# Kernel tuning notes

Hardware: AMD Instinct MI355X
Metric: run time of the kernel (lower is better)

## Reference

```python
import jax, jax.numpy as jnp
import numpy as np

N_QUERIES = 33_554_432  # 32M query points (128 MB fp32)
N_KNOTS = 1024          # interpolation table size


def setup_inputs() -> dict:
    key = jax.random.key(0)
    k1, k2, k3 = jax.random.split(key, 3)
    # queries spread slightly beyond the knot range to exercise clamping branches
    x = jax.random.uniform(k1, (N_QUERIES,), dtype=jnp.float32, minval=-0.1, maxval=1.1)
    # unsorted knots (module sorts them in __init__; reference sorts too)
    x_points = jax.random.uniform(k2, (N_KNOTS,), dtype=jnp.float32)
    y_points = jax.random.normal(k3, (N_KNOTS,), dtype=jnp.float32)
    return {"x": x, "x_points": x_points, "y_points": y_points}


def reference(x, x_points, y_points):
    # __init__: sort knots by x, permute y accordingly
    order = jnp.argsort(x_points)
    xp = x_points[order]
    yp = y_points[order]
    n = xp.shape[0]
    # torch.searchsorted default (right=False) == side='left'
    idx = jnp.searchsorted(xp, x, side="left")  # [N], int
    # interior lerp uses (idx-1, idx); clip so gathers are in-range
    hi = jnp.clip(idx, 1, n - 1)
    lo = hi - 1
    x1, x2 = xp[lo], xp[hi]
    y1, y2 = yp[lo], yp[hi]
    interp = y1 + (x - x1) * (y2 - y1) / (x2 - x1)
    # boundary clamps: idx==0 -> y[0]; idx>=n -> y[-1]
    out = jnp.where(idx == 0, yp[0], jnp.where(idx >= n, yp[-1], interp))
    return out
```

## Files before the change

kernel.cpp:

```cpp
#include <hip/hip_runtime.h>
#include <math.h>

#define NK 1024
#define NB 4096

#define WS_SXP   0
#define WS_META  1032
#define WS_QUAD  1040
#define WS_FTAB  5136

typedef float f4v __attribute__((ext_vector_type(4)));

__device__ __forceinline__ int bucket_of(float x, float lo, float scale) {
    float t = __fmul_rn(__fsub_rn(x, lo), scale);
    int b = (int)t;
    b = b < 0 ? 0 : b;
    b = b > (NB - 1) ? (NB - 1) : b;
    return b;
}

__global__ __launch_bounds__(1024) void setup_sort(
        const float* __restrict__ xp_in, const float* __restrict__ yp_in,
        float* __restrict__ wsf)
{
    __shared__ unsigned long long kl[NK];
    __shared__ float sxs[NK];
    __shared__ float sys[NK];

    const int t = threadIdx.x;

    float xv = xp_in[t];
    unsigned int fb  = __float_as_uint(xv);
    unsigned int k32 = (fb & 0x80000000u) ? ~fb : (fb | 0x80000000u);
    unsigned long long key = ((unsigned long long)k32 << 10) | (unsigned int)t;

    for (int k = 2; k <= NK; k <<= 1) {
        const bool dir = ((t & k) == 0);
        for (int j = k >> 1; j >= 64; j >>= 1) {
            kl[t] = key;
            __syncthreads();
            unsigned long long p = kl[t ^ j];
            __syncthreads();
            bool lower = ((t & j) == 0);
            bool wmin  = (dir == lower);
            unsigned long long mn = key < p ? key : p;
            unsigned long long mx = key < p ? p : key;
            key = wmin ? mn : mx;
        }
        for (int j = ((k >> 1) >= 64 ? 32 : (k >> 1)); j >= 1; j >>= 1) {
            unsigned long long p = __shfl_xor(key, j, 64);
            bool lower = ((t & j) == 0);
            bool wmin  = (dir == lower);
            unsigned long long mn = key < p ? key : p;
            unsigned long long mx = key < p ? p : key;
            key = wmin ? mn : mx;
        }
    }

    unsigned int idx0 = (unsigned int)(key & (NK - 1));
    unsigned int s32  = (unsigned int)(key >> 10);
    unsigned int xb   = (s32 & 0x80000000u) ? (s32 ^ 0x80000000u) : ~s32;
    float xs = __uint_as_float(xb);
    float ys = yp_in[idx0];
    sxs[t] = xs; sys[t] = ys;
    __syncthreads();

    float xn = (t < NK - 1) ? sxs[t + 1] : xs;
    float yn = (t < NK - 1) ? sys[t + 1] : ys;
    float slope = (t < NK - 1) ? (yn - ys) / (xn - xs) : 0.0f;

    wsf[WS_SXP + t] = xs;
    if (t < 8) wsf[WS_SXP + NK + t] = INFINITY;
    ((float4*)(wsf + WS_QUAD))[t] = make_float4(xs, ys, slope, 0.0f);
    if (t == 0) {
        float lo  = sxs[0];
        float xpN = sxs[NK - 1];
        float range = xpN - lo;
        wsf[WS_META + 0] = lo;
        wsf[WS_META + 1] = range * (1.0f / (float)NB);
        wsf[WS_META + 2] = (range > 0.0f) ? ((float)NB / range) : 0.0f;
        wsf[WS_META + 3] = sys[0];
        wsf[WS_META + 4] = sys[NK - 1];
        wsf[WS_META + 5] = xpN;
    }
}

__global__ __launch_bounds__(256) void setup_tables(float* __restrict__ wsf)
{
    __shared__ float sxp_s[NK];
    __shared__ int   lb[257];
    __shared__ float meta[6];

    const int tid = threadIdx.x;
    for (int i = tid; i < NK; i += 256) sxp_s[i] = wsf[WS_SXP + i];
    if (tid < 6) meta[tid] = wsf[WS_META + tid];
    __syncthreads();

    const float lo = meta[0], inv_scale = meta[1], scale = meta[2];
    const int base = blockIdx.x * 256;

    auto lbf = [&](int b) -> int {
        int loi = 0, hii = NK;
        while (loi < hii) {
            int mid = (loi + hii) >> 1;
            if (bucket_of(sxp_s[mid], lo, scale) < b) loi = mid + 1; else hii = mid;
        }
        return loi;
    };
    lb[tid] = lbf(base + tid);
    if (tid == 0) lb[256] = (base + 256 >= NB) ? NK : lbf(base + 256);
    __syncthreads();

    const int b   = base + tid;
    const int ib  = lb[tid];
    const int ib1 = lb[tid + 1];
    const int interior = ib1 - ib - (b == 0 ? 1 : 0) - (b == NB - 1 ? 1 : 0);

    float2 e;
    if (interior > 0) {
        e.x = __uint_as_float(0x7fc00000u);
        e.y = __uint_as_float((unsigned int)ib);
    } else {
        int hi = ib < 1 ? 1 : (ib > NK - 1 ? NK - 1 : ib);
        float4 qd = ((const float4*)(wsf + WS_QUAD))[hi - 1];
        float bl = __fmaf_rn((float)b, inv_scale, lo);
        e.x = qd.z;
        e.y = __fmaf_rn(bl - qd.x, qd.z, qd.y);
    }
    ((float2*)(wsf + WS_FTAB))[b] = e;
}

__device__ __forceinline__ float interp_one(
        float x, const float2* __restrict__ ftab, const float* __restrict__ sxp,
        const float4* __restrict__ gquads,
        float lo, float inv_scale, float scale, float xpN, float yp0, float ypN)
{
    int b = bucket_of(x, lo, scale);
    float2 e = ftab[b];
    float bl  = __fmaf_rn((float)b, inv_scale, lo);
    float res = __fmaf_rn(x - bl, e.x, e.y);
    if (__builtin_isnan(e.x) && x > lo && x <= xpN) {
        int j = (int)__float_as_uint(e.y);
        while (sxp[j] < x) ++j;
        int hi = j < 1 ? 1 : j;
        float4 qd = gquads[hi - 1];
        res = __fmaf_rn(x - qd.x, qd.z, qd.y);
    }
    res = (x <= lo)  ? yp0 : res;
    res = (x >  xpN) ? ypN : res;
    return res;
}

__global__ __launch_bounds__(512, 8) void interp_kernel(
        const f4v* __restrict__ xq, f4v* __restrict__ out,
        const float* __restrict__ wsf, int n4)
{
    __shared__ __align__(16) float2 ftab[NB];
    __shared__ float sxp_s[NK + 8];
    const int t = threadIdx.x;
    {
        const f4v* src = (const f4v*)(wsf + WS_FTAB);
        f4v*       dst = (f4v*)ftab;
        #pragma unroll
        for (int i = 0; i < 4; ++i) dst[t + 512 * i] = src[t + 512 * i];
        for (int i = t; i < NK + 8; i += 512) sxp_s[i] = wsf[WS_SXP + i];
    }
    const float lo        = wsf[WS_META + 0];
    const float inv_scale = wsf[WS_META + 1];
    const float scale     = wsf[WS_META + 2];
    const float yp0       = wsf[WS_META + 3];
    const float ypN       = wsf[WS_META + 4];
    const float xpN       = wsf[WS_META + 5];
    const float4* gquads  = (const float4*)(wsf + WS_QUAD);
    __syncthreads();

    int q = blockIdx.x * 512 + t;
    const int stride = gridDim.x * 512;
    for (; q + stride < n4; q += 2 * stride) {
        f4v xa = xq[q];
        f4v xb = xq[q + stride];
        f4v ra, rb;
        ra.x = interp_one(xa.x, ftab, sxp_s, gquads, lo, inv_scale, scale, xpN, yp0, ypN);
        ra.y = interp_one(xa.y, ftab, sxp_s, gquads, lo, inv_scale, scale, xpN, yp0, ypN);
        ra.z = interp_one(xa.z, ftab, sxp_s, gquads, lo, inv_scale, scale, xpN, yp0, ypN);
        ra.w = interp_one(xa.w, ftab, sxp_s, gquads, lo, inv_scale, scale, xpN, yp0, ypN);
        rb.x = interp_one(xb.x, ftab, sxp_s, gquads, lo, inv_scale, scale, xpN, yp0, ypN);
        rb.y = interp_one(xb.y, ftab, sxp_s, gquads, lo, inv_scale, scale, xpN, yp0, ypN);
        rb.z = interp_one(xb.z, ftab, sxp_s, gquads, lo, inv_scale, scale, xpN, yp0, ypN);
        rb.w = interp_one(xb.w, ftab, sxp_s, gquads, lo, inv_scale, scale, xpN, yp0, ypN);
        __builtin_nontemporal_store(ra, &out[q]);
        __builtin_nontemporal_store(rb, &out[q + stride]);
    }
    for (; q < n4; q += stride) {
        f4v xa = xq[q];
        f4v ra;
        ra.x = interp_one(xa.x, ftab, sxp_s, gquads, lo, inv_scale, scale, xpN, yp0, ypN);
        ra.y = interp_one(xa.y, ftab, sxp_s, gquads, lo, inv_scale, scale, xpN, yp0, ypN);
        ra.z = interp_one(xa.z, ftab, sxp_s, gquads, lo, inv_scale, scale, xpN, yp0, ypN);
        ra.w = interp_one(xa.w, ftab, sxp_s, gquads, lo, inv_scale, scale, xpN, yp0, ypN);
        __builtin_nontemporal_store(ra, &out[q]);
    }
}

extern "C" void kernel_launch(void* const* d_in, const int* in_sizes, int n_in,
                              void* d_out, int out_size, void* d_ws, size_t ws_size,
                              hipStream_t stream)
{
    const float* x  = (const float*)d_in[0];
    const float* xp = (const float*)d_in[1];
    const float* yp = (const float*)d_in[2];
    float* out = (float*)d_out;
    float* wsf = (float*)d_ws;

    setup_sort<<<1, 1024, 0, stream>>>(xp, yp, wsf);
    setup_tables<<<NB / 256, 256, 0, stream>>>(wsf);

    const int n4 = out_size / 4;
    interp_kernel<<<1024, 512, 0, stream>>>((const f4v*)x, (f4v*)out, wsf, n4);
}
```

Baseline: 262.3 us.

## Batch interpolation lookups for ILP and stage segment quads in LDS

Replaces the per-element interp_one with a templated batch routine. It issues all bucket-table loads for 8 (or 4) elements first, then runs three branch-free search steps before a residual while-loop. The per-segment quad table now lives in shared memory instead of being read from global memory, and the grid and launch bounds are reduced (768 blocks, min 6 waves). The aim is more memory-level and LDS-level parallelism and less divergent global gathers. The cost is extra LDS per block, which lowers resident blocks, plus unconditional LDS reads for lanes that need no search.

```diff
diff --git a/kernel.cpp b/kernel.cpp
--- a/kernel.cpp
+++ b/kernel.cpp
@@ -130,40 +130,71 @@
     ((float2*)(wsf + WS_FTAB))[b] = e;
 }
 
-__device__ __forceinline__ float interp_one(
-        float x, const float2* __restrict__ ftab, const float* __restrict__ sxp,
-        const float4* __restrict__ gquads,
+template<int U>
+__device__ __forceinline__ void interp_batch(
+        const float* xin, float* rout,
+        const float2* __restrict__ ftab, const float* __restrict__ sxp,
+        const float4* __restrict__ squad,
         float lo, float inv_scale, float scale, float xpN, float yp0, float ypN)
 {
-    int b = bucket_of(x, lo, scale);
-    float2 e = ftab[b];
-    float bl  = __fmaf_rn((float)b, inv_scale, lo);
-    float res = __fmaf_rn(x - bl, e.x, e.y);
-    if (__builtin_isnan(e.x) && x > lo && x <= xpN) {
-        int j = (int)__float_as_uint(e.y);
-        while (sxp[j] < x) ++j;
-        int hi = j < 1 ? 1 : j;
-        float4 qd = gquads[hi - 1];
-        res = __fmaf_rn(x - qd.x, qd.z, qd.y);
-    }
-    res = (x <= lo)  ? yp0 : res;
-    res = (x >  xpN) ? ypN : res;
-    return res;
-}
-
-__global__ __launch_bounds__(512, 8) void interp_kernel(
+    float2 e[U];
+    float  res[U];
+    int    j[U];
+    bool   fb[U];
+
+    #pragma unroll
+    for (int u = 0; u < U; ++u) {
+        int b = bucket_of(xin[u], lo, scale);
+        e[u] = ftab[b];
+        float bl = __fmaf_rn((float)b, inv_scale, lo);
+        res[u] = bl;
+    }
+    #pragma unroll
+    for (int u = 0; u < U; ++u) {
+        float bl = res[u];
+        res[u] = __fmaf_rn(xin[u] - bl, e[u].x, e[u].y);
+        fb[u]  = __builtin_isnan(e[u].x) && (xin[u] > lo) && (xin[u] <= xpN);
+        j[u]   = fb[u] ? (int)__float_as_uint(e[u].y) : 0;
+    }
+    #pragma unroll
+    for (int r = 0; r < 3; ++r) {
+        #pragma unroll
+        for (int u = 0; u < U; ++u) j[u] += (sxp[j[u]] < xin[u]) ? 1 : 0;
+    }
+    #pragma unroll
+    for (int u = 0; u < U; ++u)
+        while (fb[u] && sxp[j[u]] < xin[u]) ++j[u];
+    #pragma unroll
+    for (int u = 0; u < U; ++u) {
+        int hi = j[u] < 1 ? 1 : j[u];
+        float4 qd = squad[hi - 1];
+        float rf  = __fmaf_rn(xin[u] - qd.x, qd.z, qd.y);
+        res[u] = fb[u] ? rf : res[u];
+        res[u] = (xin[u] <= lo)  ? yp0 : res[u];
+        res[u] = (xin[u] >  xpN) ? ypN : res[u];
+        rout[u] = res[u];
+    }
+}
+
+__global__ __launch_bounds__(512, 6) void interp_kernel(
         const f4v* __restrict__ xq, f4v* __restrict__ out,
         const float* __restrict__ wsf, int n4)
 {
     __shared__ __align__(16) float2 ftab[NB];
-    __shared__ float sxp_s[NK + 8];
+    __shared__ __align__(16) float4 squad[NK];
+    __shared__ float sxp_s[NK];
     const int t = threadIdx.x;
     {
-        const f4v* src = (const f4v*)(wsf + WS_FTAB);
-        f4v*       dst = (f4v*)ftab;
-        #pragma unroll
-        for (int i = 0; i < 4; ++i) dst[t + 512 * i] = src[t + 512 * i];
-        for (int i = t; i < NK + 8; i += 512) sxp_s[i] = wsf[WS_SXP + i];
+        const f4v* fsrc = (const f4v*)(wsf + WS_FTAB);
+        f4v*       fdst = (f4v*)ftab;
+        #pragma unroll
+        for (int i = 0; i < 4; ++i) fdst[t + 512 * i] = fsrc[t + 512 * i];
+        const f4v* qsrc = (const f4v*)(wsf + WS_QUAD);
+        f4v*       qdst = (f4v*)squad;
+        #pragma unroll
+        for (int i = 0; i < 2; ++i) qdst[t + 512 * i] = qsrc[t + 512 * i];
+        #pragma unroll
+        for (int i = 0; i < 2; ++i) sxp_s[t + 512 * i] = wsf[WS_SXP + t + 512 * i];
     }
     const float lo        = wsf[WS_META + 0];
     const float inv_scale = wsf[WS_META + 1];
@@ -171,7 +202,6 @@
     const float yp0       = wsf[WS_META + 3];
     const float ypN       = wsf[WS_META + 4];
     const float xpN       = wsf[WS_META + 5];
-    const float4* gquads  = (const float4*)(wsf + WS_QUAD);
     __syncthreads();
 
     int q = blockIdx.x * 512 + t;
@@ -179,25 +209,22 @@
     for (; q + stride < n4; q += 2 * stride) {
         f4v xa = xq[q];
         f4v xb = xq[q + stride];
-        f4v ra, rb;
-        ra.x = interp_one(xa.x, ftab, sxp_s, gquads, lo, inv_scale, scale, xpN, yp0, ypN);
-        ra.y = interp_one(xa.y, ftab, sxp_s, gquads, lo, inv_scale, scale, xpN, yp0, ypN);
-        ra.z = interp_one(xa.z, ftab, sxp_s, gquads, lo, inv_scale, scale, xpN, yp0, ypN);
-        ra.w = interp_one(xa.w, ftab, sxp_s, gquads, lo, inv_scale, scale, xpN, yp0, ypN);
-        rb.x = interp_one(xb.x, ftab, sxp_s, gquads, lo, inv_scale, scale, xpN, yp0, ypN);
-        rb.y = interp_one(xb.y, ftab, sxp_s, gquads, lo, inv_scale, scale, xpN, yp0, ypN);
-        rb.z = interp_one(xb.z, ftab, sxp_s, gquads, lo, inv_scale, scale, xpN, yp0, ypN);
-        rb.w = interp_one(xb.w, ftab, sxp_s, gquads, lo, inv_scale, scale, xpN, yp0, ypN);
+        float xin[8] = {xa.x, xa.y, xa.z, xa.w, xb.x, xb.y, xb.z, xb.w};
+        float r8[8];
+        interp_batch<8>(xin, r8, ftab, sxp_s, squad,
+                        lo, inv_scale, scale, xpN, yp0, ypN);
+        f4v ra = {r8[0], r8[1], r8[2], r8[3]};
+        f4v rb = {r8[4], r8[5], r8[6], r8[7]};
         __builtin_nontemporal_store(ra, &out[q]);
         __builtin_nontemporal_store(rb, &out[q + stride]);
     }
     for (; q < n4; q += stride) {
         f4v xa = xq[q];
-        f4v ra;
-        ra.x = interp_one(xa.x, ftab, sxp_s, gquads, lo, inv_scale, scale, xpN, yp0, ypN);
-        ra.y = interp_one(xa.y, ftab, sxp_s, gquads, lo, inv_scale, scale, xpN, yp0, ypN);
-        ra.z = interp_one(xa.z, ftab, sxp_s, gquads, lo, inv_scale, scale, xpN, yp0, ypN);
-        ra.w = interp_one(xa.w, ftab, sxp_s, gquads, lo, inv_scale, scale, xpN, yp0, ypN);
+        float xin[4] = {xa.x, xa.y, xa.z, xa.w};
+        float r4[4];
+        interp_batch<4>(xin, r4, ftab, sxp_s, squad,
+                        lo, inv_scale, scale, xpN, yp0, ypN);
+        f4v ra = {r4[0], r4[1], r4[2], r4[3]};
         __builtin_nontemporal_store(ra, &out[q]);
     }
 }
@@ -216,5 +243,5 @@
     setup_tables<<<NB / 256, 256, 0, stream>>>(wsf);
 
     const int n4 = out_size / 4;
-    interp_kernel<<<1024, 512, 0, stream>>>((const f4v*)x, (f4v*)out, wsf, n4);
-}
+    interp_kernel<<<768, 512, 0, stream>>>((const f4v*)x, (f4v*)out, wsf, n4);
+}
```

Result: no change. 259.5 us (-1.1%).

## Resolve single-knot buckets directly via float4 table entries and restructure interp loop

Applied to the files above, without the earlier changes.

Widens the per-bucket lookup table to float4 so a bucket holding exactly one knot stores the knot position, its y, and the slopes on either side. Queries in such buckets pick a slope with one compare instead of taking the divergent linear-scan fallback. Only buckets with two or more knots keep the scan, which should cut wave divergence in what appears to be a compute-bound kernel. In exchange, LDS per block doubles to about 68 KB and the workspace table grows. The main loop now uses 1024-thread blocks, a register prefetch of the next input vector, and batched table lookups.

```diff
diff --git a/kernel.cpp b/kernel.cpp
--- a/kernel.cpp
+++ b/kernel.cpp
@@ -77,11 +77,10 @@
         float xpN = sxs[NK - 1];
         float range = xpN - lo;
         wsf[WS_META + 0] = lo;
-        wsf[WS_META + 1] = range * (1.0f / (float)NB);
-        wsf[WS_META + 2] = (range > 0.0f) ? ((float)NB / range) : 0.0f;
-        wsf[WS_META + 3] = sys[0];
-        wsf[WS_META + 4] = sys[NK - 1];
-        wsf[WS_META + 5] = xpN;
+        wsf[WS_META + 1] = (range > 0.0f) ? ((float)NB / range) : 0.0f;
+        wsf[WS_META + 2] = sys[0];
+        wsf[WS_META + 3] = sys[NK - 1];
+        wsf[WS_META + 4] = xpN;
     }
 }
 
@@ -89,14 +88,14 @@
 {
     __shared__ float sxp_s[NK];
     __shared__ int   lb[257];
-    __shared__ float meta[6];
+    __shared__ float meta[5];
 
     const int tid = threadIdx.x;
     for (int i = tid; i < NK; i += 256) sxp_s[i] = wsf[WS_SXP + i];
-    if (tid < 6) meta[tid] = wsf[WS_META + tid];
-    __syncthreads();
-
-    const float lo = meta[0], inv_scale = meta[1], scale = meta[2];
+    if (tid < 5) meta[tid] = wsf[WS_META + tid];
+    __syncthreads();
+
+    const float lo = meta[0], scale = meta[1];
     const int base = blockIdx.x * 256;
 
     auto lbf = [&](int b) -> int {
@@ -114,91 +113,92 @@
     const int b   = base + tid;
     const int ib  = lb[tid];
     const int ib1 = lb[tid + 1];
-    const int interior = ib1 - ib - (b == 0 ? 1 : 0) - (b == NB - 1 ? 1 : 0);
-
-    float2 e;
-    if (interior > 0) {
-        e.x = __uint_as_float(0x7fc00000u);
-        e.y = __uint_as_float((unsigned int)ib);
+    const int cnt = ib1 - ib - (b == 0 ? 1 : 0) - (b == NB - 1 ? 1 : 0);
+
+    const float4* gq = (const float4*)(wsf + WS_QUAD);
+    float4 e;
+    if (cnt <= 0) {
+        int hi = ib < 1 ? 1 : (ib > NK - 1 ? NK - 1 : ib);
+        float4 qd = gq[hi - 1];
+        e = make_float4(qd.x, qd.y, qd.z, qd.z);
+    } else if (cnt == 1) {
+        int s = ib + (b == 0 ? 1 : 0);
+        float4 qs = gq[s];
+        float4 qm = gq[s - 1];
+        e = make_float4(qs.x, qs.y, qm.z, qs.z);
     } else {
-        int hi = ib < 1 ? 1 : (ib > NK - 1 ? NK - 1 : ib);
-        float4 qd = ((const float4*)(wsf + WS_QUAD))[hi - 1];
-        float bl = __fmaf_rn((float)b, inv_scale, lo);
-        e.x = qd.z;
-        e.y = __fmaf_rn(bl - qd.x, qd.z, qd.y);
-    }
-    ((float2*)(wsf + WS_FTAB))[b] = e;
-}
-
-__device__ __forceinline__ float interp_one(
-        float x, const float2* __restrict__ ftab, const float* __restrict__ sxp,
-        const float4* __restrict__ gquads,
-        float lo, float inv_scale, float scale, float xpN, float yp0, float ypN)
-{
-    int b = bucket_of(x, lo, scale);
-    float2 e = ftab[b];
-    float bl  = __fmaf_rn((float)b, inv_scale, lo);
-    float res = __fmaf_rn(x - bl, e.x, e.y);
-    if (__builtin_isnan(e.x) && x > lo && x <= xpN) {
-        int j = (int)__float_as_uint(e.y);
-        while (sxp[j] < x) ++j;
-        int hi = j < 1 ? 1 : j;
-        float4 qd = gquads[hi - 1];
-        res = __fmaf_rn(x - qd.x, qd.z, qd.y);
-    }
-    res = (x <= lo)  ? yp0 : res;
-    res = (x >  xpN) ? ypN : res;
-    return res;
-}
-
-__global__ __launch_bounds__(512, 8) void interp_kernel(
+        e = make_float4(0.0f, 0.0f, __uint_as_float(0x7fc00000u),
+                        __uint_as_float((unsigned int)ib));
+    }
+    ((float4*)(wsf + WS_FTAB))[b] = e;
+}
+
+__global__ __launch_bounds__(1024, 8) void interp_kernel(
         const f4v* __restrict__ xq, f4v* __restrict__ out,
         const float* __restrict__ wsf, int n4)
 {
-    __shared__ __align__(16) float2 ftab[NB];
+    __shared__ __align__(16) f4v  ftab[NB];
     __shared__ float sxp_s[NK + 8];
     const int t = threadIdx.x;
     {
-        const f4v* src = (const f4v*)(wsf + WS_FTAB);
-        f4v*       dst = (f4v*)ftab;
-        #pragma unroll
-        for (int i = 0; i < 4; ++i) dst[t + 512 * i] = src[t + 512 * i];
-        for (int i = t; i < NK + 8; i += 512) sxp_s[i] = wsf[WS_SXP + i];
-    }
-    const float lo        = wsf[WS_META + 0];
-    const float inv_scale = wsf[WS_META + 1];
-    const float scale     = wsf[WS_META + 2];
-    const float yp0       = wsf[WS_META + 3];
-    const float ypN       = wsf[WS_META + 4];
-    const float xpN       = wsf[WS_META + 5];
-    const float4* gquads  = (const float4*)(wsf + WS_QUAD);
-    __syncthreads();
-
-    int q = blockIdx.x * 512 + t;
-    const int stride = gridDim.x * 512;
-    for (; q + stride < n4; q += 2 * stride) {
-        f4v xa = xq[q];
-        f4v xb = xq[q + stride];
-        f4v ra, rb;
-        ra.x = interp_one(xa.x, ftab, sxp_s, gquads, lo, inv_scale, scale, xpN, yp0, ypN);
-        ra.y = interp_one(xa.y, ftab, sxp_s, gquads, lo, inv_scale, scale, xpN, yp0, ypN);
-        ra.z = interp_one(xa.z, ftab, sxp_s, gquads, lo, inv_scale, scale, xpN, yp0, ypN);
-        ra.w = interp_one(xa.w, ftab, sxp_s, gquads, lo, inv_scale, scale, xpN, yp0, ypN);
-        rb.x = interp_one(xb.x, ftab, sxp_s, gquads, lo, inv_scale, scale, xpN, yp0, ypN);
-        rb.y = interp_one(xb.y, ftab, sxp_s, gquads, lo, inv_scale, scale, xpN, yp0, ypN);
-        rb.z = interp_one(xb.z, ftab, sxp_s, gquads, lo, inv_scale, scale, xpN, yp0, ypN);
-        rb.w = interp_one(xb.w, ftab, sxp_s, gquads, lo, inv_scale, scale, xpN, yp0, ypN);
-        __builtin_nontemporal_store(ra, &out[q]);
-        __builtin_nontemporal_store(rb, &out[q + stride]);
-    }
-    for (; q < n4; q += stride) {
-        f4v xa = xq[q];
-        f4v ra;
-        ra.x = interp_one(xa.x, ftab, sxp_s, gquads, lo, inv_scale, scale, xpN, yp0, ypN);
-        ra.y = interp_one(xa.y, ftab, sxp_s, gquads, lo, inv_scale, scale, xpN, yp0, ypN);
-        ra.z = interp_one(xa.z, ftab, sxp_s, gquads, lo, inv_scale, scale, xpN, yp0, ypN);
-        ra.w = interp_one(xa.w, ftab, sxp_s, gquads, lo, inv_scale, scale, xpN, yp0, ypN);
-        __builtin_nontemporal_store(ra, &out[q]);
+        const f4v* fsrc = (const f4v*)(wsf + WS_FTAB);
+        #pragma unroll
+        for (int i = 0; i < 4; ++i) ftab[t + 1024 * i] = fsrc[t + 1024 * i];
+        sxp_s[t] = wsf[WS_SXP + t];
+        if (t < 8) sxp_s[NK + t] = INFINITY;
+    }
+    const float lo    = wsf[WS_META + 0];
+    const float scale = wsf[WS_META + 1];
+    const float yp0   = wsf[WS_META + 2];
+    const float ypN   = wsf[WS_META + 3];
+    const float xpN   = wsf[WS_META + 4];
+    const float4* gquads = (const float4*)(wsf + WS_QUAD);
+    __syncthreads();
+
+    const int stride = gridDim.x * 1024;
+    int q = blockIdx.x * 1024 + t;
+    if (q >= n4) return;
+
+    f4v xc = xq[q];
+    for (;;) {
+        const int qn = q + stride;
+        const bool more = qn < n4;
+        f4v xn = more ? xq[qn] : xc;
+
+        float xin[4] = {xc.x, xc.y, xc.z, xc.w};
+        f4v ed[4];
+        #pragma unroll
+        for (int u = 0; u < 4; ++u) {
+            int b = bucket_of(xin[u], lo, scale);
+            ed[u] = ftab[b];
+        }
+        float res[4];
+        bool  fb[4];
+        #pragma unroll
+        for (int u = 0; u < 4; ++u) {
+            float a = (xin[u] < ed[u].x) ? ed[u].z : ed[u].w;
+            res[u]  = __fmaf_rn(xin[u] - ed[u].x, a, ed[u].y);
+            fb[u]   = __builtin_isnan(ed[u].z) && (xin[u] > lo) && (xin[u] <= xpN);
+        }
+        #pragma unroll
+        for (int u = 0; u < 4; ++u) {
+            if (fb[u]) {
+                int j = (int)__float_as_uint(ed[u].w);
+                while (sxp_s[j] < xin[u]) ++j;
+                float4 qd = gquads[j - 1];
+                res[u] = __fmaf_rn(xin[u] - qd.x, qd.z, qd.y);
+            }
+        }
+        #pragma unroll
+        for (int u = 0; u < 4; ++u) {
+            res[u] = (xin[u] <= lo)  ? yp0 : res[u];
+            res[u] = (xin[u] >  xpN) ? ypN : res[u];
+        }
+        f4v r = {res[0], res[1], res[2], res[3]};
+        __builtin_nontemporal_store(r, &out[q]);
+
+        if (!more) break;
+        xc = xn; q = qn;
     }
 }
 
@@ -216,5 +216,5 @@
     setup_tables<<<NB / 256, 256, 0, stream>>>(wsf);
 
     const int n4 = out_size / 4;
-    interp_kernel<<<1024, 512, 0, stream>>>((const f4v*)x, (f4v*)out, wsf, n4);
-}
+    interp_kernel<<<512, 1024, 0, stream>>>((const f4v*)x, (f4v*)out, wsf, n4);
+}
```

Result: faster. 254.6 us (-2.9%).
